# Optimization experiments

Hardware: AMD Instinct MI355X
Metric: run time of the kernel (lower is better)

Reference implementation:

```python
import jax, jax.numpy as jnp
import numpy as np

PAD = 1          # kernel offsets lie in [-1, 1] for kernel_size=3
COORD_MAX = 128  # coordinates quantized to [0, 128)
S = COORD_MAX + 2 * PAD  # per-dimension encoding stride (130)


def setup_inputs() -> dict:
    key = jax.random.key(0)
    B, N, D = 4, 50000, 3
    coordinates = jax.random.randint(
        jax.random.fold_in(key, 0), (B, N, D), 0, COORD_MAX, dtype=jnp.int32)
    # batch_indices[b, n] == b, matching how the torch code partitions rows
    batch_indices = jnp.broadcast_to(jnp.arange(B, dtype=jnp.int32)[:, None], (B, N))
    # 3^3 hypercube kernel offsets, lexicographic order (KernelGenerator semantics)
    r = jnp.arange(-1, 2, dtype=jnp.int32)
    kernel_offsets = jnp.stack(jnp.meshgrid(r, r, r, indexing='ij'), axis=-1).reshape(-1, 3)
    return {"coordinates": coordinates, "batch_indices": batch_indices,
            "kernel_offsets": kernel_offsets}


def reference(coordinates, batch_indices, kernel_offsets):
    """Vectorized equivalent of LocalSelfAttention.compute_kernel_mapping.

    Returns (input_idx, output_idx, rel_pos_idx, output_key_tensor, num_unique).
    The first three are [B, N, K] (the torch kernel_map flattened row-major is
    exactly zip of these), output_key_tensor is [L, D] padded with -1 beyond
    num_unique rows, with unique keys in first-occurrence (insertion) order --
    identical to the Python dict-hashing loop.
    """
    B, N, D = coordinates.shape
    K = kernel_offsets.shape[0]
    L = B * N * K

    # neighbor coords per (point, offset): [B, N, K, D]
    nb = coordinates[:, :, None, :] + kernel_offsets[None, None, :, :]

    # encode (batch_id, neighbor_coord) into a single int32 key
    enc = jnp.broadcast_to(batch_indices[:, :, None], (B, N, K)).astype(jnp.int32)
    for d in range(D):
        enc = enc * S + (nb[..., d] + PAD)  # max ~ 4*130^3 < 2^31
    keys = enc.reshape(L)

    # sort-based dedup preserving first-occurrence order
    order = jnp.argsort(keys, stable=True)              # [L]
    sk = keys[order]
    new_group = jnp.concatenate([jnp.ones((1,), bool), sk[1:] != sk[:-1]])
    gid_sorted = jnp.cumsum(new_group.astype(jnp.int32)) - 1  # group id per sorted slot
    num_unique = gid_sorted[-1] + 1

    # first flat position where each group's key occurs (empty groups -> int32 max)
    first_occ = jax.ops.segment_min(order, gid_sorted, num_segments=L)
    # insertion-order index of each group (padded groups stably rank last)
    group_rank = jnp.argsort(jnp.argsort(first_occ))

    # scatter group ids back to original flat order, then map to insertion rank
    gid = jnp.zeros((L,), jnp.int32).at[order].set(gid_sorted)
    output_idx = group_rank[gid].reshape(B, N, K).astype(jnp.int32)

    # representative encoded key per group, reordered to insertion order
    rep_key = jax.ops.segment_min(sk, gid_sorted, num_segments=L)
    enc_ord = jnp.zeros((L,), keys.dtype).at[group_rank].set(rep_key)

    # decode neighbor coordinates (drop the batch component, as torch does)
    coords_dec = []
    e = enc_ord
    for _ in range(D):
        coords_dec.append(e % S - PAD)
        e = e // S
    out_coords = jnp.stack(coords_dec[::-1], axis=-1)  # [L, D]
    valid = (jnp.arange(L) < num_unique)[:, None]
    output_key_tensor = jnp.where(valid, out_coords, -1)

    input_idx = jnp.broadcast_to(jnp.arange(N, dtype=jnp.int32)[None, :, None], (B, N, K))
    rel_pos_idx = jnp.broadcast_to(jnp.arange(K, dtype=jnp.int32)[None, None, :], (B, N, K))
    return (input_idx, output_idx, rel_pos_idx, output_key_tensor, num_unique)
```

## Files before the change

kernel.cpp:

```cpp
#include <hip/hip_runtime.h>
#include <cstdint>

#define B_   4
#define N_   50000
#define K_   27
#define P_   (B_ * N_)
#define L_   (P_ * K_)
#define S_   130
#define KS_  (B_ * S_ * S_ * S_)
#define W_   (L_ / 64)
#define NBW  ((W_ + 255) / 256)

__device__ __forceinline__ int key_of(int l, const int* __restrict__ coords,
                                      const int* __restrict__ bidx,
                                      const int* __restrict__ koffs) {
    int p = l / K_;
    int k = l - p * K_;
    int key = bidx[p];
    #pragma unroll
    for (int d = 0; d < 3; ++d) {
        int c = coords[p * 3 + d] + koffs[k * 3 + d] + 1;
        key = key * S_ + c;
    }
    return key;
}

__global__ __launch_bounds__(256) void k_init(int* __restrict__ T) {
    int i = blockIdx.x * blockDim.x + threadIdx.x;
    if (i < KS_) T[i] = 0x7fffffff;
}

__global__ __launch_bounds__(256) void k_first_fill(const int* __restrict__ coords,
                                                    const int* __restrict__ bidx,
                                                    const int* __restrict__ koffs,
                                                    int* __restrict__ T,
                                                    int* __restrict__ out0,
                                                    int* __restrict__ out2,
                                                    int* __restrict__ outkey) {
    int l = blockIdx.x * blockDim.x + threadIdx.x;
    if (l >= L_) return;
    int p = l / K_;
    int k = l - p * K_;
    out0[l] = p - (p / N_) * N_;
    out2[l] = k;
    outkey[3 * l + 0] = -1;
    outkey[3 * l + 1] = -1;
    outkey[3 * l + 2] = -1;
    int key = bidx[p];
    #pragma unroll
    for (int d = 0; d < 3; ++d)
        key = key * S_ + (coords[p * 3 + d] + koffs[k * 3 + d] + 1);
    atomicMin(&T[key], l);
}

__global__ __launch_bounds__(256) void k_flag_bitmap(const int* __restrict__ coords,
                                                     const int* __restrict__ bidx,
                                                     const int* __restrict__ koffs,
                                                     const int* __restrict__ T,
                                                     int* __restrict__ mArr,
                                                     unsigned long long* __restrict__ bitmap) {
    int l = blockIdx.x * blockDim.x + threadIdx.x;
    if (l >= L_) return;
    int key = key_of(l, coords, bidx, koffs);
    int m = T[key];
    mArr[l] = m;
    unsigned long long b = __ballot(m == l);
    if ((threadIdx.x & 63) == 0) bitmap[l >> 6] = b;
}

__global__ __launch_bounds__(256) void k_scan_words(const unsigned long long* __restrict__ bitmap,
                                                    int* __restrict__ wpre,
                                                    int* __restrict__ bsum) {
    __shared__ int sh[256];
    int w = blockIdx.x * 256 + threadIdx.x;
    int c = (w < W_) ? __popcll(bitmap[w]) : 0;
    sh[threadIdx.x] = c;
    __syncthreads();
    for (int off = 1; off < 256; off <<= 1) {
        int t = (threadIdx.x >= off) ? sh[threadIdx.x - off] : 0;
        __syncthreads();
        sh[threadIdx.x] += t;
        __syncthreads();
    }
    if (w < W_) wpre[w] = sh[threadIdx.x] - c;
    if (threadIdx.x == 255) bsum[blockIdx.x] = sh[255];
}

__global__ __launch_bounds__(512) void k_scan_block(int* __restrict__ bsum,
                                                    int* __restrict__ num_unique_out) {
    __shared__ int sh[512];
    int i = threadIdx.x;
    int v = (i < NBW) ? bsum[i] : 0;
    sh[i] = v;
    __syncthreads();
    for (int off = 1; off < 512; off <<= 1) {
        int t = (i >= off) ? sh[i - off] : 0;
        __syncthreads();
        sh[i] += t;
        __syncthreads();
    }
    if (i < NBW) bsum[i] = sh[i] - v;
    if (i == 0) num_unique_out[0] = sh[511];
}

__global__ __launch_bounds__(256) void k_finalize(const int* __restrict__ coords,
                                                  const int* __restrict__ koffs,
                                                  const unsigned long long* __restrict__ bitmap,
                                                  const int* __restrict__ wpre,
                                                  const int* __restrict__ bsum,
                                                  int* __restrict__ out1,
                                                  int* __restrict__ outkey) {
    int l = blockIdx.x * blockDim.x + threadIdx.x;
    if (l >= L_) return;
    int m = out1[l];
    int w = m >> 6;
    unsigned long long word = bitmap[w];
    unsigned long long mask = (1ull << (m & 63)) - 1ull;
    int rank = wpre[w] + bsum[w >> 8] + (int)__popcll(word & mask);
    if (m == l) {
        int p = l / K_;
        int k = l - p * K_;
        outkey[3 * rank + 0] = coords[p * 3 + 0] + koffs[k * 3 + 0];
        outkey[3 * rank + 1] = coords[p * 3 + 1] + koffs[k * 3 + 1];
        outkey[3 * rank + 2] = coords[p * 3 + 2] + koffs[k * 3 + 2];
    }
    out1[l] = rank;
}

extern "C" void kernel_launch(void* const* d_in, const int* in_sizes, int n_in,
                              void* d_out, int out_size, void* d_ws, size_t ws_size,
                              hipStream_t stream) {
    const int* coords = (const int*)d_in[0];
    const int* bidx   = (const int*)d_in[1];
    const int* koffs  = (const int*)d_in[2];

    int* out      = (int*)d_out;
    int* out0     = out;
    int* out1     = out + L_;
    int* out2     = out + 2 * L_;
    int* outkey   = out + 3 * L_;
    int* numuniq  = out + 6 * L_;

    int* T = (int*)d_ws;
    unsigned long long* bitmap = (unsigned long long*)(T + KS_);
    int* wpre = (int*)(bitmap + W_);
    int* bsum = wpre + W_;

    k_init        <<<(KS_ + 255) / 256, 256, 0, stream>>>(T);
    k_first_fill  <<<(L_ + 255) / 256, 256, 0, stream>>>(coords, bidx, koffs, T, out0, out2, outkey);
    k_flag_bitmap <<<(L_ + 255) / 256, 256, 0, stream>>>(coords, bidx, koffs, T, out1, bitmap);
    k_scan_words  <<<NBW, 256, 0, stream>>>(bitmap, wpre, bsum);
    k_scan_block  <<<1, 512, 0, stream>>>(bsum, numuniq);
    k_finalize    <<<(L_ + 255) / 256, 256, 0, stream>>>(coords, koffs, bitmap, wpre, bsum, out1, outkey);
}
```

Baseline: 156.9 us.

## Replace per-neighbor atomicMin scatter with point table plus separable min-dilation

```diff
diff --git a/kernel.cpp b/kernel.cpp
--- a/kernel.cpp
+++ b/kernel.cpp
@@ -7,65 +7,91 @@
 #define P_   (B_ * N_)
 #define L_   (P_ * K_)
 #define S_   130
-#define KS_  (B_ * S_ * S_ * S_)
+#define PL_  (S_ * S_)
+#define BB_  (S_ * S_ * S_)
+#define KS_  (B_ * BB_)
 #define W_   (L_ / 64)
 #define NBW  ((W_ + 255) / 256)
+#define BIG_ 0x7f000000
 
-__device__ __forceinline__ int key_of(int l, const int* __restrict__ coords,
-                                      const int* __restrict__ bidx,
-                                      const int* __restrict__ koffs) {
-    int p = l / K_;
-    int k = l - p * K_;
-    int key = bidx[p];
-    #pragma unroll
-    for (int d = 0; d < 3; ++d) {
-        int c = coords[p * 3 + d] + koffs[k * 3 + d] + 1;
-        key = key * S_ + c;
+__global__ __launch_bounds__(256) void k_init_fill(int* __restrict__ P1,
+                                                   int* __restrict__ out0,
+                                                   int* __restrict__ out2) {
+    int i = blockIdx.x * blockDim.x + threadIdx.x;
+    if (i < KS_) P1[i] = BIG_;
+    if (i < L_) {
+        int p = i / K_;
+        int k = i - p * K_;
+        out0[i] = p - (p / N_) * N_;
+        out2[i] = k;
     }
-    return key;
 }
 
-__global__ __launch_bounds__(256) void k_init(int* __restrict__ T) {
-    int i = blockIdx.x * blockDim.x + threadIdx.x;
-    if (i < KS_) T[i] = 0x7fffffff;
+__global__ __launch_bounds__(256) void k_ptab(const int* __restrict__ coords,
+                                              const int* __restrict__ bidx,
+                                              int* __restrict__ P1) {
+    int p = blockIdx.x * blockDim.x + threadIdx.x;
+    if (p >= P_) return;
+    int b = bidx[p];
+    int x = coords[3 * p + 0] + 1;
+    int y = coords[3 * p + 1] + 1;
+    int z = coords[3 * p + 2] + 1;
+    int idx = ((b * S_ + x) * S_ + y) * S_ + z;
+    atomicMin(&P1[idx], p << 5);
 }
 
-__global__ __launch_bounds__(256) void k_first_fill(const int* __restrict__ coords,
-                                                    const int* __restrict__ bidx,
-                                                    const int* __restrict__ koffs,
-                                                    int* __restrict__ T,
-                                                    int* __restrict__ out0,
-                                                    int* __restrict__ out2,
-                                                    int* __restrict__ outkey) {
-    int l = blockIdx.x * blockDim.x + threadIdx.x;
-    if (l >= L_) return;
-    int p = l / K_;
-    int k = l - p * K_;
-    out0[l] = p - (p / N_) * N_;
-    out2[l] = k;
-    outkey[3 * l + 0] = -1;
-    outkey[3 * l + 1] = -1;
-    outkey[3 * l + 2] = -1;
-    int key = bidx[p];
-    #pragma unroll
-    for (int d = 0; d < 3; ++d)
-        key = key * S_ + (coords[p * 3 + d] + koffs[k * 3 + d] + 1);
-    atomicMin(&T[key], l);
+__global__ __launch_bounds__(256) void k_minz(const int* __restrict__ src,
+                                              int* __restrict__ dst) {
+    int i = blockIdx.x * blockDim.x + threadIdx.x;
+    if (i >= KS_) return;
+    int z = i % S_;
+    int v = src[i] + 1;
+    if (z > 0)      v = min(v, src[i - 1] + 2);
+    if (z < S_ - 1) v = min(v, src[i + 1]);
+    dst[i] = v;
+}
+
+__global__ __launch_bounds__(256) void k_miny(const int* __restrict__ src,
+                                              int* __restrict__ dst) {
+    int i = blockIdx.x * blockDim.x + threadIdx.x;
+    if (i >= KS_) return;
+    int y = (i / S_) % S_;
+    int v = src[i] + 3;
+    if (y > 0)      v = min(v, src[i - S_] + 6);
+    if (y < S_ - 1) v = min(v, src[i + S_]);
+    dst[i] = v;
+}
+
+__global__ __launch_bounds__(256) void k_minx(const int* __restrict__ src,
+                                              int* __restrict__ dst) {
+    int i = blockIdx.x * blockDim.x + threadIdx.x;
+    if (i >= KS_) return;
+    int x = (i / PL_) % S_;
+    int v = src[i] + 9;
+    if (x > 0)      v = min(v, src[i - PL_] + 18);
+    if (x < S_ - 1) v = min(v, src[i + PL_]);
+    dst[i] = v;
 }
 
 __global__ __launch_bounds__(256) void k_flag_bitmap(const int* __restrict__ coords,
                                                      const int* __restrict__ bidx,
                                                      const int* __restrict__ koffs,
-                                                     const int* __restrict__ T,
+                                                     const int* __restrict__ M,
                                                      int* __restrict__ mArr,
                                                      unsigned long long* __restrict__ bitmap) {
     int l = blockIdx.x * blockDim.x + threadIdx.x;
     if (l >= L_) return;
-    int key = key_of(l, coords, bidx, koffs);
-    int m = T[key];
-    mArr[l] = m;
-    unsigned long long b = __ballot(m == l);
-    if ((threadIdx.x & 63) == 0) bitmap[l >> 6] = b;
+    int p = l / K_;
+    int k = l - p * K_;
+    int b = bidx[p];
+    int cx = coords[3 * p + 0] + koffs[3 * k + 0] + 1;
+    int cy = coords[3 * p + 1] + koffs[3 * k + 1] + 1;
+    int cz = coords[3 * p + 2] + koffs[3 * k + 2] + 1;
+    int idx = ((b * S_ + cx) * S_ + cy) * S_ + cz;
+    int m32 = M[idx];
+    mArr[l] = m32;
+    unsigned long long bal = __ballot(m32 == ((p << 5) | k));
+    if ((threadIdx.x & 63) == 0) bitmap[l >> 6] = bal;
 }
 
 __global__ __launch_bounds__(256) void k_scan_words(const unsigned long long* __restrict__ bitmap,
@@ -108,11 +134,13 @@
                                                   const unsigned long long* __restrict__ bitmap,
                                                   const int* __restrict__ wpre,
                                                   const int* __restrict__ bsum,
+                                                  const int* __restrict__ numuniq,
                                                   int* __restrict__ out1,
                                                   int* __restrict__ outkey) {
     int l = blockIdx.x * blockDim.x + threadIdx.x;
     if (l >= L_) return;
-    int m = out1[l];
+    int m32 = out1[l];
+    int m = (m32 >> 5) * K_ + (m32 & 31);
     int w = m >> 6;
     unsigned long long word = bitmap[w];
     unsigned long long mask = (1ull << (m & 63)) - 1ull;
@@ -120,11 +148,16 @@
     if (m == l) {
         int p = l / K_;
         int k = l - p * K_;
-        outkey[3 * rank + 0] = coords[p * 3 + 0] + koffs[k * 3 + 0];
-        outkey[3 * rank + 1] = coords[p * 3 + 1] + koffs[k * 3 + 1];
-        outkey[3 * rank + 2] = coords[p * 3 + 2] + koffs[k * 3 + 2];
+        outkey[3 * rank + 0] = coords[3 * p + 0] + koffs[3 * k + 0];
+        outkey[3 * rank + 1] = coords[3 * p + 1] + koffs[3 * k + 1];
+        outkey[3 * rank + 2] = coords[3 * p + 2] + koffs[3 * k + 2];
     }
     out1[l] = rank;
+    if (l >= numuniq[0]) {
+        outkey[3 * l + 0] = -1;
+        outkey[3 * l + 1] = -1;
+        outkey[3 * l + 2] = -1;
+    }
 }
 
 extern "C" void kernel_launch(void* const* d_in, const int* in_sizes, int n_in,
@@ -141,15 +174,21 @@
     int* outkey   = out + 3 * L_;
     int* numuniq  = out + 6 * L_;
 
-    int* T = (int*)d_ws;
-    unsigned long long* bitmap = (unsigned long long*)(T + KS_);
+    int* P1 = (int*)d_ws;
+    unsigned long long* bitmap = (unsigned long long*)(P1 + KS_);
     int* wpre = (int*)(bitmap + W_);
     int* bsum = wpre + W_;
 
-    k_init        <<<(KS_ + 255) / 256, 256, 0, stream>>>(T);
-    k_first_fill  <<<(L_ + 255) / 256, 256, 0, stream>>>(coords, bidx, koffs, T, out0, out2, outkey);
-    k_flag_bitmap <<<(L_ + 255) / 256, 256, 0, stream>>>(coords, bidx, koffs, T, out1, bitmap);
+    int* A = outkey;
+
+    k_init_fill   <<<(KS_ + 255) / 256, 256, 0, stream>>>(P1, out0, out2);
+    k_ptab        <<<(P_ + 255) / 256, 256, 0, stream>>>(coords, bidx, P1);
+    k_minz        <<<(KS_ + 255) / 256, 256, 0, stream>>>(P1, A);
+    k_miny        <<<(KS_ + 255) / 256, 256, 0, stream>>>(A, P1);
+    k_minx        <<<(KS_ + 255) / 256, 256, 0, stream>>>(P1, A);
+    k_flag_bitmap <<<(L_ + 255) / 256, 256, 0, stream>>>(coords, bidx, koffs, A, out1, bitmap);
     k_scan_words  <<<NBW, 256, 0, stream>>>(bitmap, wpre, bsum);
     k_scan_block  <<<1, 512, 0, stream>>>(bsum, numuniq);
-    k_finalize    <<<(L_ + 255) / 256, 256, 0, stream>>>(coords, koffs, bitmap, wpre, bsum, out1, outkey);
+    k_finalize    <<<(L_ + 255) / 256, 256, 0, stream>>>(coords, koffs, bitmap, wpre, bsum,
+                                                         numuniq, out1, outkey);
 }
```

Result: slower. 162.6 us (+3.6%).
